# Optimization experiments

Hardware: AMD Instinct MI355X
Metric: run time of the kernel (lower is better)

## Reference

```python
import jax, jax.numpy as jnp
import numpy as np

B, Hm, Wm, Dm = 1, 32, 32, 32
N = Hm * Wm * Dm
C = 128
HEADS, DH = 8, 16
G = 32
L = 2
OUT = 1


def _ln(x, g, b):
    mu = jnp.mean(x, -1, keepdims=True)
    var = jnp.mean((x - mu) ** 2, -1, keepdims=True)
    return (x - mu) * jax.lax.rsqrt(var + 1e-5) * g + b


def setup_inputs() -> dict:
    key = jax.random.key(0)
    ks = iter(jax.random.split(key, 64))
    def nrm(shape, s=0.02):
        return jax.random.normal(next(ks), shape, jnp.float32) * s
    return {
        "x": jax.random.normal(next(ks), (B, N, 3), jnp.float32),
        "fx": jax.random.normal(next(ks), (B, N, 1), jnp.float32),
        "pre_w1": nrm((4, 2 * C)), "pre_b1": jnp.zeros((2 * C,), jnp.float32),
        "pre_w2": nrm((2 * C, C)), "pre_b2": jnp.zeros((C,), jnp.float32),
        "placeholder": jax.random.uniform(next(ks), (C,), jnp.float32) / C,
        "ln1_g": jnp.ones((L, C), jnp.float32), "ln1_b": jnp.zeros((L, C), jnp.float32),
        "convx_w": nrm((L, C, C, 3, 3, 3)), "convx_b": jnp.zeros((L, C), jnp.float32),
        "convfx_w": nrm((L, C, C, 3, 3, 3)), "convfx_b": jnp.zeros((L, C), jnp.float32),
        "slice_w": nrm((L, DH, G), 0.1), "slice_b": jnp.zeros((L, G), jnp.float32),
        "temperature": jnp.full((L, 1, HEADS, 1, 1), 0.5, jnp.float32),
        "wq": nrm((L, DH, DH), 0.1), "wk": nrm((L, DH, DH), 0.1), "wv": nrm((L, DH, DH), 0.1),
        "wo": nrm((L, HEADS * DH, C)), "bo": jnp.zeros((L, C), jnp.float32),
        "ln2_g": jnp.ones((L, C), jnp.float32), "ln2_b": jnp.zeros((L, C), jnp.float32),
        "mlp_w1": nrm((L, C, C)), "mlp_b1": jnp.zeros((L, C), jnp.float32),
        "mlp_w2": nrm((L, C, C)), "mlp_b2": jnp.zeros((L, C), jnp.float32),
        "ln3_g": jnp.ones((C,), jnp.float32), "ln3_b": jnp.zeros((C,), jnp.float32),
        "out_w": nrm((C, OUT)), "out_b": jnp.zeros((OUT,), jnp.float32),
    }


def _conv3d(x, w, b):
    # x: [B,C,H,W,D], w: [O,I,3,3,3], SAME padding (kernel//2) as torch Conv3d
    y = jax.lax.conv_general_dilated(x, w, (1, 1, 1), "SAME",
                                     dimension_numbers=("NCDHW", "OIDHW", "NCDHW"))
    return y + b[None, :, None, None, None]


def _physics_attn(z, cw_x, cb_x, cw_fx, cb_fx, sw, sb, temp, wq, wk, wv, wo, bo):
    # z: [B, N, C] -> structured mesh conv projections -> slice attention
    xg = z.reshape(B, Hm, Wm, Dm, C).transpose(0, 4, 1, 2, 3)  # [B,C,H,W,D]

    def split_heads(t):  # [B,I,H,W,D] -> [B,heads,N,dh]
        return t.transpose(0, 2, 3, 4, 1).reshape(B, N, HEADS, DH).transpose(0, 2, 1, 3)

    x_mid = split_heads(_conv3d(xg, cw_x, cb_x))
    fx_mid = split_heads(_conv3d(xg, cw_fx, cb_fx))
    # slice assignment weights: [B,heads,N,G], temperature-scaled softmax
    slice_logits = (x_mid @ sw + sb) / temp
    swt = jax.nn.softmax(slice_logits, axis=-1)
    norm = jnp.sum(swt, axis=2)  # [B,heads,G]
    tok = jnp.einsum("bhnc,bhng->bhgc", fx_mid, swt) / (norm + 1e-5)[..., None]
    q, k, v = tok @ wq, tok @ wk, tok @ wv  # [B,heads,G,dh]
    attn = jax.nn.softmax((q @ k.transpose(0, 1, 3, 2)) * (DH ** -0.5), axis=-1)
    ot = attn @ v  # [B,heads,G,dh]
    out = jnp.einsum("bhgc,bhng->bhnc", ot, swt)  # de-slice back to tokens
    out = out.transpose(0, 2, 1, 3).reshape(B, N, HEADS * DH)
    return out @ wo + bo


def reference(x, fx, pre_w1, pre_b1, pre_w2, pre_b2, placeholder,
              ln1_g, ln1_b, convx_w, convx_b, convfx_w, convfx_b,
              slice_w, slice_b, temperature, wq, wk, wv, wo, bo,
              ln2_g, ln2_b, mlp_w1, mlp_b1, mlp_w2, mlp_b2,
              ln3_g, ln3_b, out_w, out_b):
    h = jnp.concatenate([x, fx], axis=-1)  # [B,N,space+fun]
    z = jax.nn.gelu(h @ pre_w1 + pre_b1, approximate=False) @ pre_w2 + pre_b2 + placeholder
    for l in range(L):
        zn = _ln(z, ln1_g[l], ln1_b[l])
        z = _physics_attn(zn, convx_w[l], convx_b[l], convfx_w[l], convfx_b[l],
                          slice_w[l], slice_b[l], temperature[l],
                          wq[l], wk[l], wv[l], wo[l], bo[l]) + z
        zn = _ln(z, ln2_g[l], ln2_b[l])
        z = jax.nn.gelu(zn @ mlp_w1[l] + mlp_b1[l], approximate=False) @ mlp_w2[l] + mlp_b2[l] + z
    return _ln(z, ln3_g, ln3_b) @ out_w + out_b
```

## Files before the change

### kernel.cpp

```cpp
#include <hip/hip_runtime.h>
#include <hip/hip_bf16.h>

#define DEV __device__ __forceinline__

constexpr int N   = 32768;
constexpr int TOTAL_IN = 2038481;

constexpr int OFF_X        = 0;
constexpr int OFF_FX       = 98304;
constexpr int OFF_PRE_W1   = 131072;
constexpr int OFF_PRE_B1   = 132096;
constexpr int OFF_PRE_W2   = 132352;
constexpr int OFF_PRE_B2   = 165120;
constexpr int OFF_PLACE    = 165248;
constexpr int OFF_LN1_G    = 165376;
constexpr int OFF_LN1_B    = 165632;
constexpr int OFF_CONVX_W  = 165888;
constexpr int OFF_CONVX_B  = 1050624;
constexpr int OFF_CONVFX_W = 1050880;
constexpr int OFF_CONVFX_B = 1935616;
constexpr int OFF_SLICE_W  = 1935872;
constexpr int OFF_SLICE_B  = 1936896;
constexpr int OFF_TEMP     = 1936960;
constexpr int OFF_WQ       = 1936976;
constexpr int OFF_WK       = 1937488;
constexpr int OFF_WV       = 1938000;
constexpr int OFF_WO       = 1938512;
constexpr int OFF_BO       = 1971280;
constexpr int OFF_LN2_G    = 1971536;
constexpr int OFF_LN2_B    = 1971792;
constexpr int OFF_MLP_W1   = 1972048;
constexpr int OFF_MLP_B1   = 2004816;
constexpr int OFF_MLP_W2   = 2005072;
constexpr int OFF_MLP_B2   = 2037840;
constexpr int OFF_LN3_G    = 2038096;
constexpr int OFF_LN3_B    = 2038224;
constexpr int OFF_OUT_W    = 2038352;
constexpr int OFF_OUT_B    = 2038480;

__device__ __constant__ int d_PRE[32] = {
  0, 98304, 131072, 132096, 132352, 165120, 165248, 165376, 165632,
  165888, 1050624, 1050880, 1935616, 1935872, 1936896, 1936960, 1936976,
  1937488, 1938000, 1938512, 1971280, 1971536, 1971792, 1972048, 2004816,
  2005072, 2037840, 2038096, 2038224, 2038352, 2038480, 2038481
};

constexpr size_t F_IN   = 16;
constexpr size_t F_WT   = 2038512;
constexpr size_t F_Z    = F_WT   + 1769472;
constexpr size_t F_ZN   = F_Z    + 4194304;
constexpr size_t F_CONV = F_ZN   + 4194304;
constexpr size_t F_SWT  = F_CONV + 8388608;
constexpr size_t F_TOKP = F_SWT  + 8388608;
constexpr size_t F_TOK2 = F_TOKP + 1114112;
constexpr size_t F_WP   = F_TOK2 + 34816;
constexpr size_t F_END  = F_WP   + 65536;

struct InPtrs { const void* p[31]; };

typedef short short8v  __attribute__((ext_vector_type(8)));
typedef float float4v  __attribute__((ext_vector_type(4)));
#define MFMA16(A,B,C) __builtin_amdgcn_mfma_f32_16x16x32_bf16(A,B,C,0,0,0)

DEV float geluf(float x) { return 0.5f * x * (1.0f + erff(x * 0.70710678118654752f)); }
DEV short f2bs(float x) { union { __hip_bfloat16 h; short s; } c; c.h = __float2bfloat16(x); return c.s; }
DEV float bs2f(short s) { union { unsigned u; float f; } c; c.u = ((unsigned)(unsigned short)s) << 16; return c.f; }

__global__ void k_setup(InPtrs ptrs, float* __restrict__ ws,
                        short* __restrict__ wtf, short* __restrict__ wp) {
  __shared__ short wl[13952];
  const bool isbf = (*(const unsigned*)ptrs.p[15] == 0x3F003F00u);
  int b = blockIdx.x, tid = threadIdx.x;
  if (b < 512) {
    int stride = 512 * 256;
    for (int e = b * 256 + tid; e < TOTAL_IN; e += stride) {
      if ((e >= OFF_CONVX_W && e < OFF_CONVX_B) || (e >= OFF_CONVFX_W && e < OFF_CONVFX_B)) continue;
      int lo = 0, hi = 30;
#pragma unroll
      for (int it = 0; it < 5; ++it) {
        int mid = (lo + hi + 1) >> 1;
        if (e >= d_PRE[mid]) lo = mid; else hi = mid - 1;
      }
      int loc = e - d_PRE[lo];
      float v;
      if (isbf) {
        unsigned short u = ((const unsigned short*)ptrs.p[lo])[loc];
        v = __uint_as_float(((unsigned)u) << 16);
      } else {
        v = ((const float*)ptrs.p[lo])[loc];
      }
      ws[F_IN + e] = v;
    }
  } else if (b < 640) {
    int idx = b - 512;
    int layer = idx >> 6, rem = idx & 63;
    int icb = rem >> 4, ntile = rem & 15;
    for (int i = tid; i < 13824; i += 256) {
      int oc_r = i / 864, off = i - oc_r * 864;
      int oc = ntile * 16 + oc_r;
      const void* cw = (oc < 128) ? ptrs.p[9] : ptrs.p[11];
      size_t base = ((size_t)(layer * 128 + (oc & 127)) * 128 + icb * 32) * 27 + off;
      wl[oc_r * 872 + off] = isbf ? (short)((const unsigned short*)cw)[base]
                                  : f2bs(((const float*)cw)[base]);
    }
    __syncthreads();
    int wv = tid >> 6, lane = tid & 63;
    int m = lane & 15, q = lane >> 4;
    for (int tg = 0; tg < 7; ++tg) {
      int tap = tg * 4 + wv;
      if (tap < 27) {
        short8v out;
#pragma unroll
        for (int j = 0; j < 8; ++j) out[j] = wl[m * 872 + (q * 8 + j) * 27 + tap];
        size_t f = ((size_t)((layer * 108 + icb * 27 + tap) * 16 + ntile)) * 64 + lane;
        *(short8v*)(wtf + f * 8) = out;
      }
    }
  } else {
    int f = (b - 640) * 256 + tid;
    int lane = f & 63;
    int t = f >> 6;
    const void* srcb; size_t soff; int kt, nt;
    if (t < 64) { srcb = ptrs.p[4]; soff = 0; kt = t >> 3; nt = t & 7; }
    else {
      int r = t - 64, l = r / 96, r2 = r - l * 96;
      int which = r2 >> 5, idx2 = r2 & 31;
      kt = idx2 >> 3; nt = idx2 & 7;
      srcb = (which == 0 ? ptrs.p[23] : (which == 1 ? ptrs.p[25] : ptrs.p[19]));
      soff = (size_t)l * 16384;
    }
    int k0 = kt * 32 + (lane >> 4) * 8;
    int n = nt * 16 + (lane & 15);
    size_t base = soff + (size_t)k0 * 128 + n;
    short8v out;
    if (isbf) {
      const unsigned short* src = (const unsigned short*)srcb + base;
#pragma unroll
      for (int j = 0; j < 8; ++j) out[j] = (short)src[(size_t)j * 128];
    } else {
      const float* src = (const float*)srcb + base;
#pragma unroll
      for (int j = 0; j < 8; ++j) out[j] = f2bs(src[(size_t)j * 128]);
    }
    *(short8v*)(wp + (size_t)f * 8) = out;
  }
}

__global__ __launch_bounds__(256)
void k_prenet(const float* __restrict__ ip, const short* __restrict__ wp,
              float* __restrict__ z, short* __restrict__ znb) {
  __shared__ float w1s[1024], b1s[256], cvec[128], g1s[128], be1s[128];
  __shared__ float xv[64][4];
  __shared__ __align__(16) short ts[64 * 264];
  int tid = threadIdx.x;
  int wv = tid >> 6, lane = tid & 63;
  int m = lane & 15, q = lane >> 4;
  int n0 = blockIdx.x * 64;
  for (int i = tid; i < 1024; i += 256) w1s[i] = ip[OFF_PRE_W1 + i];
  b1s[tid] = ip[OFF_PRE_B1 + tid];
  if (tid < 128) {
    cvec[tid] = ip[OFF_PRE_B2 + tid] + ip[OFF_PLACE + tid];
    g1s[tid]  = ip[OFF_LN1_G + tid];
    be1s[tid] = ip[OFF_LN1_B + tid];
  }
  if (tid < 64) {
    xv[tid][0] = ip[OFF_X + (n0 + tid) * 3 + 0];
    xv[tid][1] = ip[OFF_X + (n0 + tid) * 3 + 1];
    xv[tid][2] = ip[OFF_X + (n0 + tid) * 3 + 2];
    xv[tid][3] = ip[OFF_FX + n0 + tid];
  }
  __syncthreads();
  {
    float w0 = w1s[tid], wA = w1s[256 + tid], wB = w1s[512 + tid], wC = w1s[768 + tid];
    float bb = b1s[tid];
    for (int t = 0; t < 64; ++t) {
      float hv = bb + xv[t][0] * w0 + xv[t][1] * wA + xv[t][2] * wB + xv[t][3] * wC;
      ts[t * 264 + tid] = f2bs(geluf(hv));
    }
  }
  __syncthreads();
  const short8v* pwf = (const short8v*)wp;
  float4v acc[8];
#pragma unroll
  for (int nt = 0; nt < 8; ++nt) acc[nt] = (float4v){0.f, 0.f, 0.f, 0.f};
  for (int kt = 0; kt < 8; ++kt) {
    short8v A = *(const short8v*)(ts + (wv * 16 + m) * 264 + kt * 32 + q * 8);
#pragma unroll
    for (int nt = 0; nt < 8; ++nt)
      acc[nt] = MFMA16(A, pwf[(kt * 8 + nt) * 64 + lane], acc[nt]);
  }
  float vz[8][4];
#pragma unroll
  for (int nt = 0; nt < 8; ++nt) {
    int col = nt * 16 + m;
#pragma unroll
    for (int r = 0; r < 4; ++r) {
      vz[nt][r] = acc[nt][r] + cvec[col];
      z[(size_t)(n0 + wv * 16 + q * 4 + r) * 128 + col] = vz[nt][r];
    }
  }
#pragma unroll
  for (int r = 0; r < 4; ++r) {
    float s1 = 0.f, s2 = 0.f;
#pragma unroll
    for (int nt = 0; nt < 8; ++nt) { float v = vz[nt][r]; s1 += v; s2 += v * v; }
#pragma unroll
    for (int off = 1; off < 16; off <<= 1) { s1 += __shfl_xor(s1, off); s2 += __shfl_xor(s2, off); }
    float mu = s1 * (1.0f / 128.0f);
    float var = s2 * (1.0f / 128.0f) - mu * mu;
    float rst = 1.0f / sqrtf(var + 1e-5f);
    size_t rowb = (size_t)(n0 + wv * 16 + q * 4 + r) * 128;
#pragma unroll
    for (int nt = 0; nt < 8; ++nt) {
      int col = nt * 16 + m;
      znb[rowb + col] = f2bs((vz[nt][r] - mu) * rst * g1s[col] + be1s[col]);
    }
  }
}

__global__ __launch_bounds__(256)
void k_conv(const float* __restrict__ ip, const short* __restrict__ znb,
            const short* __restrict__ wtf, short* __restrict__ cvb, int layer) {
  __shared__ __align__(16) short halo[30720];
  int tid = threadIdx.x;
  int wv = tid >> 6, lane = tid & 63;
  int m = lane & 15, q = lane >> 4;
  int n0 = blockIdx.x * 64;
  int h = n0 >> 10, w0 = (n0 >> 5) & 31;
  float bias_r[4];
#pragma unroll
  for (int nt = 0; nt < 4; ++nt) {
    int oc = (wv * 4 + nt) * 16 + m;
    bias_r[nt] = (oc < 128) ? ip[OFF_CONVX_B + layer * 128 + oc]
                            : ip[OFF_CONVFX_B + layer * 128 + (oc - 128)];
  }
  float4v acc[4][4];
#pragma unroll
  for (int a = 0; a < 4; ++a)
#pragma unroll
    for (int b = 0; b < 4; ++b) acc[a][b] = (float4v){0.f, 0.f, 0.f, 0.f};

  const short8v* wf = (const short8v*)wtf + (size_t)layer * 110592 + (wv * 4) * 64 + lane;
  short8v bc0 = wf[0], bc1 = wf[64], bc2 = wf[128], bc3 = wf[192];

  {
    short8v tmp[7];
#pragma unroll
    for (int it = 0; it < 7; ++it) {
      int i = tid + it * 256;
      int pr = i >> 2, qq = i & 3;
      int line = pr / 34, dpos = pr - line * 34;
      int hh2 = h + (line >> 2) - 1, ww2 = w0 + (line & 3) - 1, dd2 = dpos - 1;
      short8v v = (short8v){0, 0, 0, 0, 0, 0, 0, 0};
      if (pr < 408 && ((unsigned)hh2 < 32u) && ((unsigned)ww2 < 32u) && ((unsigned)dd2 < 32u)) {
        int tok = (hh2 << 10) + (ww2 << 5) + dd2;
        v = *(const short8v*)(znb + (size_t)tok * 128 + qq * 8);
      }
      tmp[it] = v;
    }
#pragma unroll
    for (int it = 0; it < 7; ++it) {
      int i = tid + it * 256;
      int pr = i >> 2, qq = i & 3;
      int line = pr / 34, dpos = pr - line * 34;
      int off = (pr < 408) ? (qq * 3840 + (line * 40 + dpos) * 8) : 15344;
      *(short8v*)(halo + off) = tmp[it];
    }
  }
  __syncthreads();

  int tap = 0, icb = 0;
  for (int kt = 0; kt < 108; ++kt) {
    if (tap == 0 && icb < 3) {
      short* dst = halo + ((icb + 1) & 1) * 15360;
      int icn = icb + 1;
      short8v tmp[7];
#pragma unroll
      for (int it = 0; it < 7; ++it) {
        int i = tid + it * 256;
        int pr = i >> 2, qq = i & 3;
        int line = pr / 34, dpos = pr - line * 34;
        int hh2 = h + (line >> 2) - 1, ww2 = w0 + (line & 3) - 1, dd2 = dpos - 1;
        short8v v = (short8v){0, 0, 0, 0, 0, 0, 0, 0};
        if (pr < 408 && ((unsigned)hh2 < 32u) && ((unsigned)ww2 < 32u) && ((unsigned)dd2 < 32u)) {
          int tok = (hh2 << 10) + (ww2 << 5) + dd2;
          v = *(const short8v*)(znb + (size_t)tok * 128 + icn * 32 + qq * 8);
        }
        tmp[it] = v;
      }
#pragma unroll
      for (int it = 0; it < 7; ++it) {
        int i = tid + it * 256;
        int pr = i >> 2, qq = i & 3;
        int line = pr / 34, dpos = pr - line * 34;
        int off = (pr < 408) ? (qq * 3840 + (line * 40 + dpos) * 8) : 15344;
        *(short8v*)(dst + off) = tmp[it];
      }
    }
    int ktn = (kt + 1 < 108) ? kt + 1 : kt;
    const short8v* wn = wf + (size_t)ktn * 1024;
    short8v bn0 = wn[0], bn1 = wn[64], bn2 = wn[128], bn3 = wn[192];

    int ta = tap / 9, rem = tap - ta * 9, tb = rem / 3, tc = rem - tb * 3;
    const short* hp = halo + (icb & 1) * 15360 + q * 3840 + ((ta * 4 + tb) * 40 + tc + m) * 8;
    short8v A0 = *(const short8v*)(hp);
    short8v A1 = *(const short8v*)(hp + 128);
    short8v A2 = *(const short8v*)(hp + 320);
    short8v A3 = *(const short8v*)(hp + 448);

    acc[0][0] = MFMA16(A0, bc0, acc[0][0]);
    acc[1][0] = MFMA16(A1, bc0, acc[1][0]);
    acc[2][0] = MFMA16(A2, bc0, acc[2][0]);
    acc[3][0] = MFMA16(A3, bc0, acc[3][0]);
    acc[0][1] = MFMA16(A0, bc1, acc[0][1]);
    acc[1][1] = MFMA16(A1, bc1, acc[1][1]);
    acc[2][1] = MFMA16(A2, bc1, acc[2][1]);
    acc[3][1] = MFMA16(A3, bc1, acc[3][1]);
    acc[0][2] = MFMA16(A0, bc2, acc[0][2]);
    acc[1][2] = MFMA16(A1, bc2, acc[1][2]);
    acc[2][2] = MFMA16(A2, bc2, acc[2][2]);
    acc[3][2] = MFMA16(A3, bc2, acc[3][2]);
    acc[0][3] = MFMA16(A0, bc3, acc[0][3]);
    acc[1][3] = MFMA16(A1, bc3, acc[1][3]);
    acc[2][3] = MFMA16(A2, bc3, acc[2][3]);
    acc[3][3] = MFMA16(A3, bc3, acc[3][3]);

    bc0 = bn0; bc1 = bn1; bc2 = bn2; bc3 = bn3;
    if (++tap == 27) {
      tap = 0; ++icb;
      __syncthreads();
    }
  }
#pragma unroll
  for (int mt = 0; mt < 4; ++mt) {
    short* cp = cvb + (size_t)(n0 + mt * 16 + q * 4) * 256 + (wv * 4) * 16 + m;
#pragma unroll
    for (int nt = 0; nt < 4; ++nt) {
#pragma unroll
      for (int r = 0; r < 4; ++r)
        cp[(size_t)r * 256 + nt * 16] = f2bs(acc[mt][nt][r] + bias_r[nt]);
    }
  }
}

__global__ __launch_bounds__(256)
void k_slice(const float* __restrict__ ip, const short* __restrict__ cvb,
             short* __restrict__ swtb, float* __restrict__ tokp, int layer) {
  __shared__ float sws[512], sbs[32], its[8];
  __shared__ float swl[32 * 257];
  __shared__ __align__(16) short fxl[32 * 132];
  int tid = threadIdx.x;
  for (int i = tid; i < 512; i += 256) sws[i] = ip[OFF_SLICE_W + layer * 512 + i];
  if (tid < 32) sbs[tid] = ip[OFF_SLICE_B + layer * 32 + tid];
  if (tid < 8)  its[tid] = 1.0f / ip[OFF_TEMP + layer * 8 + tid];
  float4 ta0 = make_float4(0,0,0,0), ta1 = ta0, ta2 = ta0, ta3 = ta0;
  float np = 0.f;
  for (int s = 0; s < 4; ++s) {
    int tbase = blockIdx.x * 128 + s * 32;
    __syncthreads();
    for (int i = tid; i < 512; i += 256) {
      int t = i >> 4, c8 = (i & 15) * 8;
      *(short8v*)(fxl + t * 132 + c8) = *(const short8v*)(cvb + (size_t)(tbase + t) * 256 + 128 + c8);
    }
    {
      int t = tid >> 3, hh = tid & 7;
      float xm[16];
      short8v x0 = *(const short8v*)(cvb + (size_t)(tbase + t) * 256 + hh * 16);
      short8v x1 = *(const short8v*)(cvb + (size_t)(tbase + t) * 256 + hh * 16 + 8);
#pragma unroll
      for (int j = 0; j < 8; ++j) { xm[j] = bs2f(x0[j]); xm[8 + j] = bs2f(x1[j]); }
      float lg[32];
      float itv = its[hh];
#pragma unroll
      for (int g = 0; g < 32; ++g) {
        float sacc = sbs[g];
#pragma unroll
        for (int j = 0; j < 16; ++j) sacc += xm[j] * sws[j * 32 + g];
        lg[g] = sacc * itv;
      }
      float mx = -1e30f;
#pragma unroll
      for (int g = 0; g < 32; ++g) mx = fmaxf(mx, lg[g]);
      float sum = 0.f;
#pragma unroll
      for (int g = 0; g < 32; ++g) { lg[g] = expf(lg[g] - mx); sum += lg[g]; }
      float inv = 1.0f / sum;
#pragma unroll
      for (int g = 0; g < 32; ++g) {
        lg[g] *= inv;
        swl[t * 257 + hh * 32 + g] = lg[g];
      }
#pragma unroll
      for (int qq = 0; qq < 4; ++qq) {
        short8v pk;
#pragma unroll
        for (int j = 0; j < 8; ++j) pk[j] = f2bs(lg[qq * 8 + j]);
        *(short8v*)(swtb + (size_t)(tbase + t) * 256 + hh * 32 + qq * 8) = pk;
      }
    }
    __syncthreads();
    {
      int ah = tid >> 5, ag = tid & 31;
      for (int t2 = 0; t2 < 32; ++t2) {
        float sv = swl[t2 * 257 + ah * 32 + ag];
        np += sv;
        short8v f0 = *(const short8v*)(fxl + t2 * 132 + ah * 16);
        short8v f1 = *(const short8v*)(fxl + t2 * 132 + ah * 16 + 8);
        ta0.x += sv * bs2f(f0[0]); ta0.y += sv * bs2f(f0[1]); ta0.z += sv * bs2f(f0[2]); ta0.w += sv * bs2f(f0[3]);
        ta1.x += sv * bs2f(f0[4]); ta1.y += sv * bs2f(f0[5]); ta1.z += sv * bs2f(f0[6]); ta1.w += sv * bs2f(f0[7]);
        ta2.x += sv * bs2f(f1[0]); ta2.y += sv * bs2f(f1[1]); ta2.z += sv * bs2f(f1[2]); ta2.w += sv * bs2f(f1[3]);
        ta3.x += sv * bs2f(f1[4]); ta3.y += sv * bs2f(f1[5]); ta3.z += sv * bs2f(f1[6]); ta3.w += sv * bs2f(f1[7]);
      }
    }
  }
  int ah = tid >> 5, ag = tid & 31;
  size_t base = (size_t)blockIdx.x * 4352 + (size_t)(ah * 32 + ag) * 16;
  *(float4*)&tokp[base + 0]  = ta0;
  *(float4*)&tokp[base + 4]  = ta1;
  *(float4*)&tokp[base + 8]  = ta2;
  *(float4*)&tokp[base + 12] = ta3;
  tokp[(size_t)blockIdx.x * 4352 + 4096 + ah * 32 + ag] = np;
}

__global__ void k_tokred1(const float* __restrict__ tokp, float* __restrict__ tok2) {
  int ogrp = blockIdx.x % 17, bgrp = blockIdx.x / 17;
  int o = ogrp * 256 + threadIdx.x;
  float s = 0.f;
  int b0 = bgrp * 32;
#pragma unroll 8
  for (int b = b0; b < b0 + 32; ++b) s += tokp[(size_t)b * 4352 + o];
  tok2[(size_t)bgrp * 4352 + o] = s;
}

__global__ __launch_bounds__(256)
void k_fused(const float* __restrict__ ip, const short* __restrict__ swtb,
             const float* __restrict__ tok2, const short* __restrict__ wp,
             float* __restrict__ z, short* __restrict__ znb,
             void* __restrict__ dout, const void* __restrict__ tempraw, int layer) {
  __shared__ __align__(16) char smem[64512];
  short* otb = (short*)smem;
  float* bia = (float*)(smem + 8192);
  float* trs = (float*)(smem + 12288);
  short* znt = (short*)(smem + 12288);
  float* kk  = (float*)(smem + 29696);
  short* al  = (short*)(smem + 29696);
  float* vvs = (float*)(smem + 47104);
  float* bol = bia, *b1s = bia + 128, *b2s = bia + 256, *g2s = bia + 384;
  float* be2s = bia + 512, *lng = bia + 640, *lnb = bia + 768, *ows = bia + 896;
  int tid = threadIdx.x;
  int wv = tid >> 6, lane = tid & 63;
  int m = lane & 15, q = lane >> 4;
  int n0 = blockIdx.x * 64;
  if (tid < 128) {
    bol[tid]  = ip[OFF_BO + layer * 128 + tid];
    b1s[tid]  = ip[OFF_MLP_B1 + layer * 128 + tid];
    b2s[tid]  = ip[OFF_MLP_B2 + layer * 128 + tid];
    g2s[tid]  = ip[OFF_LN2_G + layer * 128 + tid];
    be2s[tid] = ip[OFF_LN2_B + layer * 128 + tid];
    if (layer == 0) {
      lng[tid] = ip[OFF_LN1_G + 128 + tid];
      lnb[tid] = ip[OFF_LN1_B + 128 + tid];
      ows[tid] = 0.f;
    } else {
      lng[tid] = ip[OFF_LN3_G + tid];
      lnb[tid] = ip[OFF_LN3_B + tid];
      ows[tid] = ip[OFF_OUT_W + tid];
    }
  }
  for (int i = tid; i < 4352; i += 256) {
    float s = 0.f;
#pragma unroll
    for (int b = 0; b < 8; ++b) s += tok2[(size_t)b * 4352 + i];
    trs[i] = s;
  }
  __syncthreads();
  float qv[16];
  {
    const float* wqp = ip + OFF_WQ + layer * 256;
    const float* wkp = ip + OFF_WK + layer * 256;
    const float* wvp = ip + OFF_WV + layer * 256;
    float inv = 1.0f / (trs[4096 + tid] + 1e-5f);
    float t[16];
#pragma unroll
    for (int c = 0; c < 16; ++c) t[c] = trs[tid * 16 + c] * inv;
#pragma unroll
    for (int c = 0; c < 16; ++c) {
      float aq = 0.f, ak = 0.f, av = 0.f;
#pragma unroll
      for (int j = 0; j < 16; ++j) {
        float tv = t[j];
        aq += tv * wqp[j * 16 + c];
        ak += tv * wkp[j * 16 + c];
        av += tv * wvp[j * 16 + c];
      }
      qv[c] = aq;
      kk[tid * 17 + c] = ak;
      vvs[tid * 17 + c] = av;
    }
  }
  __syncthreads();
  {
    int hh = tid >> 5, g = tid & 31;
    float sc[32];
    float mx = -1e30f;
#pragma unroll
    for (int g2 = 0; g2 < 32; ++g2) {
      float s = 0.f;
#pragma unroll
      for (int c = 0; c < 16; ++c) s += qv[c] * kk[(hh * 32 + g2) * 17 + c];
      s *= 0.25f;
      sc[g2] = s; mx = fmaxf(mx, s);
    }
    float sum = 0.f;
#pragma unroll
    for (int g2 = 0; g2 < 32; ++g2) { sc[g2] = expf(sc[g2] - mx); sum += sc[g2]; }
    float inv2 = 1.0f / sum;
    float o[16];
#pragma unroll
    for (int c = 0; c < 16; ++c) o[c] = 0.f;
#pragma unroll
    for (int g2 = 0; g2 < 32; ++g2) {
      float p = sc[g2] * inv2;
#pragma unroll
      for (int c = 0; c < 16; ++c) o[c] += p * vvs[(hh * 32 + g2) * 17 + c];
    }
#pragma unroll
    for (int dh = 0; dh < 16; ++dh)
      otb[hh * 512 + (((g >> 3) * 16 + dh) << 3) + (g & 7)] = f2bs(o[dh]);
  }
  __syncthreads();
  float4v accd[8];
#pragma unroll
  for (int h = 0; h < 8; ++h) accd[h] = (float4v){0.f, 0.f, 0.f, 0.f};
#pragma unroll
  for (int h = 0; h < 8; ++h) {
    short8v A = *(const short8v*)(swtb + (size_t)(n0 + wv * 16 + m) * 256 + h * 32 + q * 8);
    accd[h] = MFMA16(A, *(const short8v*)(otb + h * 512 + lane * 8), accd[h]);
  }
  __syncthreads();
#pragma unroll
  for (int h = 0; h < 8; ++h)
#pragma unroll
    for (int r = 0; r < 4; ++r)
      al[(wv * 16 + q * 4 + r) * 136 + h * 16 + m] = f2bs(accd[h][r]);
  __syncthreads();
  const short8v* wof = (const short8v*)(wp + (size_t)(128 + 96 * layer) * 512);
  float4v a2[8];
#pragma unroll
  for (int nt = 0; nt < 8; ++nt) a2[nt] = (float4v){0.f, 0.f, 0.f, 0.f};
  for (int kt = 0; kt < 4; ++kt) {
    short8v A = *(const short8v*)(al + (wv * 16 + m) * 136 + kt * 32 + q * 8);
#pragma unroll
    for (int nt = 0; nt < 8; ++nt)
      a2[nt] = MFMA16(A, wof[(kt * 8 + nt) * 64 + lane], a2[nt]);
  }
  float vmid[8][4];
#pragma unroll
  for (int nt = 0; nt < 8; ++nt) {
    int col = nt * 16 + m;
#pragma unroll
    for (int r = 0; r < 4; ++r)
      vmid[nt][r] = z[(size_t)(n0 + wv * 16 + q * 4 + r) * 128 + col] + a2[nt][r] + bol[col];
  }
#pragma unroll
  for (int r = 0; r < 4; ++r) {
    float s1 = 0.f, s2 = 0.f;
#pragma unroll
    for (int nt = 0; nt < 8; ++nt) { float v = vmid[nt][r]; s1 += v; s2 += v * v; }
#pragma unroll
    for (int off = 1; off < 16; off <<= 1) { s1 += __shfl_xor(s1, off); s2 += __shfl_xor(s2, off); }
    float mu = s1 * (1.0f / 128.0f);
    float var = s2 * (1.0f / 128.0f) - mu * mu;
    float rst = 1.0f / sqrtf(var + 1e-5f);
#pragma unroll
    for (int nt = 0; nt < 8; ++nt) {
      int col = nt * 16 + m;
      znt[(wv * 16 + q * 4 + r) * 136 + col] = f2bs((vmid[nt][r] - mu) * rst * g2s[col] + be2s[col]);
    }
  }
  __syncthreads();
  const short8v* w1f = (const short8v*)(wp + (size_t)(64 + 96 * layer) * 512);
  const short8v* w2f = (const short8v*)(wp + (size_t)(96 + 96 * layer) * 512);
  float4v acc[8];
#pragma unroll
  for (int nt = 0; nt < 8; ++nt) acc[nt] = (float4v){0.f, 0.f, 0.f, 0.f};
  for (int kt = 0; kt < 4; ++kt) {
    short8v A = *(const short8v*)(znt + (wv * 16 + m) * 136 + kt * 32 + q * 8);
#pragma unroll
    for (int nt = 0; nt < 8; ++nt)
      acc[nt] = MFMA16(A, w1f[(kt * 8 + nt) * 64 + lane], acc[nt]);
  }
  __syncthreads();
#pragma unroll
  for (int nt = 0; nt < 8; ++nt) {
    int col = nt * 16 + m;
#pragma unroll
    for (int r = 0; r < 4; ++r)
      al[(wv * 16 + q * 4 + r) * 136 + col] = f2bs(geluf(acc[nt][r] + b1s[col]));
  }
  __syncthreads();
  float4v a4[8];
#pragma unroll
  for (int nt = 0; nt < 8; ++nt) a4[nt] = (float4v){0.f, 0.f, 0.f, 0.f};
  for (int kt = 0; kt < 4; ++kt) {
    short8v A = *(const short8v*)(al + (wv * 16 + m) * 136 + kt * 32 + q * 8);
#pragma unroll
    for (int nt = 0; nt < 8; ++nt)
      a4[nt] = MFMA16(A, w2f[(kt * 8 + nt) * 64 + lane], a4[nt]);
  }
  float vfin[8][4];
#pragma unroll
  for (int nt = 0; nt < 8; ++nt) {
    int col = nt * 16 + m;
#pragma unroll
    for (int r = 0; r < 4; ++r) {
      vfin[nt][r] = vmid[nt][r] + a4[nt][r] + b2s[col];
      z[(size_t)(n0 + wv * 16 + q * 4 + r) * 128 + col] = vfin[nt][r];
    }
  }
#pragma unroll
  for (int r = 0; r < 4; ++r) {
    float s1 = 0.f, s2 = 0.f;
#pragma unroll
    for (int nt = 0; nt < 8; ++nt) { float v = vfin[nt][r]; s1 += v; s2 += v * v; }
#pragma unroll
    for (int off = 1; off < 16; off <<= 1) { s1 += __shfl_xor(s1, off); s2 += __shfl_xor(s2, off); }
    float mu = s1 * (1.0f / 128.0f);
    float var = s2 * (1.0f / 128.0f) - mu * mu;
    float rst = 1.0f / sqrtf(var + 1e-5f);
    int n = n0 + wv * 16 + q * 4 + r;
    if (layer == 0) {
      size_t rowb = (size_t)n * 128;
#pragma unroll
      for (int nt = 0; nt < 8; ++nt) {
        int col = nt * 16 + m;
        znb[rowb + col] = f2bs((vfin[nt][r] - mu) * rst * lng[col] + lnb[col]);
      }
    } else {
      float contrib = 0.f;
#pragma unroll
      for (int nt = 0; nt < 8; ++nt) {
        int col = nt * 16 + m;
        contrib += ((vfin[nt][r] - mu) * rst * lng[col] + lnb[col]) * ows[col];
      }
#pragma unroll
      for (int off = 1; off < 16; off <<= 1) contrib += __shfl_xor(contrib, off);
      if (m == 0) {
        float res = contrib + ip[OFF_OUT_B];
        unsigned tw = *(const unsigned*)tempraw;
        if (tw == 0x3F003F00u) ((__hip_bfloat16*)dout)[n] = __float2bfloat16(res);
        else                   ((float*)dout)[n] = res;
      }
    }
  }
}

extern "C" void kernel_launch(void* const* d_in, const int* in_sizes, int n_in,
                              void* d_out, int out_size, void* d_ws, size_t ws_size,
                              hipStream_t stream) {
  (void)in_sizes; (void)out_size; (void)ws_size;
  if (n_in < 31) return;
  float* ws   = (float*)d_ws;
  float* ip   = ws + F_IN;
  short* wtf  = (short*)(ws + F_WT);
  float* z    = ws + F_Z;
  short* znb  = (short*)(ws + F_ZN);
  short* cvb  = (short*)(ws + F_CONV);
  short* swtb = (short*)(ws + F_SWT);
  float* tkp  = ws + F_TOKP;
  float* tk2  = ws + F_TOK2;
  short* wp   = (short*)(ws + F_WP);

  InPtrs P;
  for (int i = 0; i < 31; ++i) P.p[i] = d_in[i];

  k_setup <<<704, 256, 0, stream>>>(P, ws, wtf, wp);
  k_prenet<<<512, 256, 0, stream>>>(ip, wp, z, znb);
  for (int l = 0; l < 2; ++l) {
    k_conv   <<<512, 256, 0, stream>>>(ip, znb, wtf, cvb, l);
    k_slice  <<<256, 256, 0, stream>>>(ip, cvb, swtb, tkp, l);
    k_tokred1<<<136, 256, 0, stream>>>(tkp, tk2);
    k_fused  <<<512, 256, 0, stream>>>(ip, swtb, tk2, wp, z, znb, d_out, d_in[15], l);
  }
}
```

Before: 435.2 us.

## Stage conv halo via direct global-to-LDS loads with a compact layout

Replaces the register-staged halo copy in the 3D conv kernel with __builtin_amdgcn_global_load_lds, which writes 16-byte chunks straight into LDS. Out-of-bounds positions read from a small zeroed buffer in the workspace. The halo layout becomes token-major (34 positions by 32 channels) with no padding, which shrinks LDS use and changes the A-fragment offsets. The goal is to cut VGPR pressure and the extra copy through registers, but the compact layout may cause LDS bank conflicts on the fragment reads. The async load may also need explicit waits before the barrier.

```diff
diff --git a/kernel.cpp b/kernel.cpp
--- a/kernel.cpp
+++ b/kernel.cpp
@@ -54,13 +54,17 @@
 constexpr size_t F_TOKP = F_SWT  + 8388608;
 constexpr size_t F_TOK2 = F_TOKP + 1114112;
 constexpr size_t F_WP   = F_TOK2 + 34816;
-constexpr size_t F_END  = F_WP   + 65536;
+constexpr size_t F_ZERO = F_WP   + 65536;
+constexpr size_t F_END  = F_ZERO + 64;
 
 struct InPtrs { const void* p[31]; };
 
 typedef short short8v  __attribute__((ext_vector_type(8)));
 typedef float float4v  __attribute__((ext_vector_type(4)));
 #define MFMA16(A,B,C) __builtin_amdgcn_mfma_f32_16x16x32_bf16(A,B,C,0,0,0)
+
+typedef const __attribute__((address_space(1))) void* gas_p;
+typedef __attribute__((address_space(3))) void* las_p;
 
 DEV float geluf(float x) { return 0.5f * x * (1.0f + erff(x * 0.70710678118654752f)); }
 DEV short f2bs(float x) { union { __hip_bfloat16 h; short s; } c; c.h = __float2bfloat16(x); return c.s; }
@@ -72,6 +76,7 @@
   const bool isbf = (*(const unsigned*)ptrs.p[15] == 0x3F003F00u);
   int b = blockIdx.x, tid = threadIdx.x;
   if (b < 512) {
+    if (b == 0 && tid < 64) ws[F_ZERO + tid] = 0.f;
     int stride = 512 * 256;
     for (int e = b * 256 + tid; e < TOTAL_IN; e += stride) {
       if ((e >= OFF_CONVX_W && e < OFF_CONVX_B) || (e >= OFF_CONVFX_W && e < OFF_CONVFX_B)) continue;
@@ -220,8 +225,9 @@
 
 __global__ __launch_bounds__(256)
 void k_conv(const float* __restrict__ ip, const short* __restrict__ znb,
-            const short* __restrict__ wtf, short* __restrict__ cvb, int layer) {
-  __shared__ __align__(16) short halo[30720];
+            const short* __restrict__ wtf, short* __restrict__ cvb,
+            const float* __restrict__ zerof, int layer) {
+  __shared__ __align__(16) short halo[26624];
   int tid = threadIdx.x;
   int wv = tid >> 6, lane = tid & 63;
   int m = lane & 15, q = lane >> 4;
@@ -243,70 +249,37 @@
   const short8v* wf = (const short8v*)wtf + (size_t)layer * 110592 + (wv * 4) * 64 + lane;
   short8v bc0 = wf[0], bc1 = wf[64], bc2 = wf[128], bc3 = wf[192];
 
-  {
-    short8v tmp[7];
-#pragma unroll
-    for (int it = 0; it < 7; ++it) {
-      int i = tid + it * 256;
-      int pr = i >> 2, qq = i & 3;
+  auto stage = [&](int icb, short* dst) {
+    for (int g = wv; g < 26; g += 4) {
+      int c = g * 64 + lane;
+      int pr = c >> 2, qq = c & 3;
       int line = pr / 34, dpos = pr - line * 34;
       int hh2 = h + (line >> 2) - 1, ww2 = w0 + (line & 3) - 1, dd2 = dpos - 1;
-      short8v v = (short8v){0, 0, 0, 0, 0, 0, 0, 0};
-      if (pr < 408 && ((unsigned)hh2 < 32u) && ((unsigned)ww2 < 32u) && ((unsigned)dd2 < 32u)) {
-        int tok = (hh2 << 10) + (ww2 << 5) + dd2;
-        v = *(const short8v*)(znb + (size_t)tok * 128 + qq * 8);
-      }
-      tmp[it] = v;
-    }
-#pragma unroll
-    for (int it = 0; it < 7; ++it) {
-      int i = tid + it * 256;
-      int pr = i >> 2, qq = i & 3;
-      int line = pr / 34, dpos = pr - line * 34;
-      int off = (pr < 408) ? (qq * 3840 + (line * 40 + dpos) * 8) : 15344;
-      *(short8v*)(halo + off) = tmp[it];
-    }
-  }
+      bool ok = (pr < 408) && ((unsigned)hh2 < 32u) && ((unsigned)ww2 < 32u) && ((unsigned)dd2 < 32u);
+      int tok = (hh2 << 10) + (ww2 << 5) + dd2;
+      const void* src = ok ? (const void*)(znb + (size_t)tok * 128 + icb * 32 + qq * 8)
+                           : (const void*)zerof;
+      __builtin_amdgcn_global_load_lds((gas_p)src, (las_p)(dst + g * 512), 16, 0, 0);
+    }
+  };
+
+  stage(0, halo);
   __syncthreads();
 
   int tap = 0, icb = 0;
   for (int kt = 0; kt < 108; ++kt) {
-    if (tap == 0 && icb < 3) {
-      short* dst = halo + ((icb + 1) & 1) * 15360;
-      int icn = icb + 1;
-      short8v tmp[7];
-#pragma unroll
-      for (int it = 0; it < 7; ++it) {
-        int i = tid + it * 256;
-        int pr = i >> 2, qq = i & 3;
-        int line = pr / 34, dpos = pr - line * 34;
-        int hh2 = h + (line >> 2) - 1, ww2 = w0 + (line & 3) - 1, dd2 = dpos - 1;
-        short8v v = (short8v){0, 0, 0, 0, 0, 0, 0, 0};
-        if (pr < 408 && ((unsigned)hh2 < 32u) && ((unsigned)ww2 < 32u) && ((unsigned)dd2 < 32u)) {
-          int tok = (hh2 << 10) + (ww2 << 5) + dd2;
-          v = *(const short8v*)(znb + (size_t)tok * 128 + icn * 32 + qq * 8);
-        }
-        tmp[it] = v;
-      }
-#pragma unroll
-      for (int it = 0; it < 7; ++it) {
-        int i = tid + it * 256;
-        int pr = i >> 2, qq = i & 3;
-        int line = pr / 34, dpos = pr - line * 34;
-        int off = (pr < 408) ? (qq * 3840 + (line * 40 + dpos) * 8) : 15344;
-        *(short8v*)(dst + off) = tmp[it];
-      }
-    }
+    if (tap == 0 && icb < 3)
+      stage(icb + 1, halo + ((icb + 1) & 1) * 13312);
     int ktn = (kt + 1 < 108) ? kt + 1 : kt;
     const short8v* wn = wf + (size_t)ktn * 1024;
     short8v bn0 = wn[0], bn1 = wn[64], bn2 = wn[128], bn3 = wn[192];
 
     int ta = tap / 9, rem = tap - ta * 9, tb = rem / 3, tc = rem - tb * 3;
-    const short* hp = halo + (icb & 1) * 15360 + q * 3840 + ((ta * 4 + tb) * 40 + tc + m) * 8;
+    const short* hp = halo + (icb & 1) * 13312 + ((ta * 4 + tb) * 34 + tc + m) * 32 + q * 8;
     short8v A0 = *(const short8v*)(hp);
-    short8v A1 = *(const short8v*)(hp + 128);
-    short8v A2 = *(const short8v*)(hp + 320);
-    short8v A3 = *(const short8v*)(hp + 448);
+    short8v A1 = *(const short8v*)(hp + 512);
+    short8v A2 = *(const short8v*)(hp + 1088);
+    short8v A3 = *(const short8v*)(hp + 1600);
 
     acc[0][0] = MFMA16(A0, bc0, acc[0][0]);
     acc[1][0] = MFMA16(A1, bc0, acc[1][0]);
@@ -670,6 +643,7 @@
   float* tkp  = ws + F_TOKP;
   float* tk2  = ws + F_TOK2;
   short* wp   = (short*)(ws + F_WP);
+  float* zf   = ws + F_ZERO;
 
   InPtrs P;
   for (int i = 0; i < 31; ++i) P.p[i] = d_in[i];
@@ -677,7 +651,7 @@
   k_setup <<<704, 256, 0, stream>>>(P, ws, wtf, wp);
   k_prenet<<<512, 256, 0, stream>>>(ip, wp, z, znb);
   for (int l = 0; l < 2; ++l) {
-    k_conv   <<<512, 256, 0, stream>>>(ip, znb, wtf, cvb, l);
+    k_conv   <<<512, 256, 0, stream>>>(ip, znb, wtf, cvb, zf, l);
     k_slice  <<<256, 256, 0, stream>>>(ip, cvb, swtb, tkp, l);
     k_tokred1<<<136, 256, 0, stream>>>(tkp, tk2);
     k_fused  <<<512, 256, 0, stream>>>(ip, swtb, tk2, wp, z, znb, d_out, d_in[15], l);
```

New measurement: 443.6 us. No clear change (+1.9%).
